# Kernel optimization log

Hardware: AMD Instinct MI355X
Metric: run time of the kernel (lower is better)

The kernel has to match this reference:

```python
import jax, jax.numpy as jnp
import numpy as np

NUM_PER_PATH = 16
MARGIN_INTRA = 0.1
MARGIN_INTER = 1.0


def setup_inputs() -> dict:
    key = jax.random.key(0)
    # [B, block_num, 1, 1, 2]; trailing dims must multiply to 2 (see _get_center view)
    path_fea = jax.random.normal(key, (131072, 64, 1, 1, 2), dtype=jnp.float32)
    return {"path_fea": path_fea}


def reference(path_fea):
    B, block = path_fea.shape[0], path_fea.shape[1]
    D = block * 2                     # flattened per-sample feature dim
    G = B // NUM_PER_PATH             # number of centers (groups)
    fea = path_fea.reshape(B, D)      # [B, D] (matches path_fea[j].view(-1))

    # center: mean over the NUM_PER_PATH samples of each group, per block
    # (identical math to the permute/view dance in _get_center)
    grouped = fea.reshape(G, NUM_PER_PATH, D)          # [G, P, D]
    center = jnp.mean(grouped, axis=1)                 # [G, D]

    # ---- inter loss: hinge on pairwise euclidean distances between centers ----
    sq = jnp.sum(center * center, axis=1)              # [G]
    gram = center @ center.T                           # [G, G]
    d2 = jnp.maximum(sq[:, None] + sq[None, :] - 2.0 * gram, 0.0)
    pair_mask = jnp.triu(jnp.ones((G, G), dtype=bool), k=1)  # i < j
    d = jnp.sqrt(jnp.where(pair_mask, d2, 1.0))        # safe sqrt off-mask
    hinge = jnp.maximum(MARGIN_INTER - d, 0.0) ** 2
    n_pairs = G * (G - 1) / 2.0
    inter_loss = jnp.sum(jnp.where(pair_mask, hinge, 0.0)) / n_pairs

    # ---- intra loss: hinge on distance of each sample to its group center ----
    diff = grouped - center[:, None, :]                # [G, P, D]
    di = jnp.sqrt(jnp.sum(diff * diff, axis=-1))       # [G, P]
    intra_loss = jnp.sum(jnp.maximum(di - MARGIN_INTRA, 0.0) ** 2) / (G * NUM_PER_PATH)

    return (inter_loss, intra_loss)
```

## Files before the change

kernel.cpp:

```cpp
#include <hip/hip_runtime.h>
#include <hip/hip_bf16.h>
#include <math.h>

#define B_ROWS   131072
#define D_DIM    128
#define P_SAMP   16
#define G_GROUPS 8192
#define TILE64   128
#define NTRI     8256
#define K1_BLOCKS (G_GROUPS / 4)

typedef __bf16 bf16x8  __attribute__((ext_vector_type(8)));
typedef float  floatx4 __attribute__((ext_vector_type(4)));
typedef unsigned short u16x8 __attribute__((ext_vector_type(8)));


__device__ __forceinline__ float wave_red64(float v) {
    #pragma unroll
    for (int off = 32; off > 0; off >>= 1) v += __shfl_xor(v, off, 64);
    return v;
}

__global__ __launch_bounds__(256) void k_center_intra(
    const float* __restrict__ x,
    uint2* __restrict__ cfrag,
    float* __restrict__ sq,
    float* __restrict__ partial,
    float* __restrict__ acc)
{
    const int wave = threadIdx.x >> 6;
    const int lane = threadIdx.x & 63;
    const int half = lane >> 5;
    const int c    = lane & 31;
    const int g    = blockIdx.x * 4 + wave;

    if (blockIdx.x == 0 && threadIdx.x == 0) acc[0] = 0.f;

    const float* base = x + (size_t)g * (P_SAMP * D_DIM) + half * D_DIM + c * 4;

    floatx4 v[8];
    #pragma unroll
    for (int l = 0; l < 8; ++l)
        v[l] = *(const floatx4*)(base + l * (2 * D_DIM));

    floatx4 cs = v[0];
    #pragma unroll
    for (int l = 1; l < 8; ++l) cs += v[l];
    #pragma unroll
    for (int k = 0; k < 4; ++k) cs[k] += __shfl_xor(cs[k], 32, 64);
    floatx4 ctr = cs * (1.0f / P_SAMP);

    float p[9];
    #pragma unroll
    for (int l = 0; l < 8; ++l) {
        floatx4 d = v[l] - ctr;
        p[l] = d[0]*d[0] + d[1]*d[1] + d[2]*d[2] + d[3]*d[3];
    }
    p[8] = ctr[0]*ctr[0] + ctr[1]*ctr[1] + ctr[2]*ctr[2] + ctr[3]*ctr[3];

    #pragma unroll
    for (int off = 16; off > 0; off >>= 1) {
        #pragma unroll
        for (int s = 0; s < 9; ++s) p[s] += __shfl_xor(p[s], off, 64);
    }

    if (half == 0) {
        unsigned int b0 = __builtin_bit_cast(unsigned short, (__bf16)ctr[0]);
        unsigned int b1 = __builtin_bit_cast(unsigned short, (__bf16)ctr[1]);
        unsigned int b2 = __builtin_bit_cast(unsigned short, (__bf16)ctr[2]);
        unsigned int b3 = __builtin_bit_cast(unsigned short, (__bf16)ctr[3]);
        uint2 pk;
        pk.x = (b1 << 16) | b0;
        pk.y = (b3 << 16) | b2;
        const int gran = (g >> 4) * 256 + (c >> 1) * 16 + (g & 15);
        cfrag[gran * 2 + (c & 1)] = pk;
    }
    if (lane == 0) sq[g] = p[8];

    float isum = 0.f;
    #pragma unroll
    for (int l = 0; l < 8; ++l) {
        float d = sqrtf(p[l]);
        float t = fmaxf(d - 0.1f, 0.f);
        isum += t * t;
    }
    isum += __shfl_xor(isum, 32, 64);

    __shared__ float sh[4];
    if (lane == 0) sh[wave] = isum;
    __syncthreads();
    if (threadIdx.x == 0)
        partial[blockIdx.x] = sh[0] + sh[1] + sh[2] + sh[3];
}

__global__ __launch_bounds__(256) void k_inter(
    const u16x8* __restrict__ cfrag,
    const float* __restrict__ sq,
    float* __restrict__ acc)
{
    const int wid  = blockIdx.x * 4 + (threadIdx.x >> 6);
    const int lane = threadIdx.x & 63;
    const int lrow = lane & 15;
    const int quad = lane >> 4;

    double s = sqrt(128.5 * 128.5 - 2.0 * (double)wid);
    int ti = (int)(128.5 - s);
    if (ti < 0) ti = 0;
    if (ti > TILE64 - 1) ti = TILE64 - 1;
    #define TRI_OFF(i) ((i) * TILE64 - (((i) * ((i) - 1)) >> 1))
    while (ti > 0 && TRI_OFF(ti) > wid) --ti;
    while (ti < TILE64 - 1 && TRI_OFF(ti + 1) <= wid) ++ti;
    const int tj = ti + (wid - TRI_OFF(ti));
    #undef TRI_OFF

    const int i0 = ti * 64;
    const int j0 = tj * 64;

    floatx4 sqi[4];
    float   sqj[4];
    #pragma unroll
    for (int mt = 0; mt < 4; ++mt)
        sqi[mt] = *(const floatx4*)(sq + i0 + mt * 16 + quad * 4);
    #pragma unroll
    for (int nt = 0; nt < 4; ++nt)
        sqj[nt] = sq[j0 + nt * 16 + lrow];

    #define FRAG_IDX(rg, ks) ((rg) * 256 + ((ks) * 4 + quad) * 16 + lrow)

    bf16x8 a[2][4], b[2][4];
    #pragma unroll
    for (int pb = 0; pb < 2; ++pb) {
        #pragma unroll
        for (int mt = 0; mt < 4; ++mt)
            a[pb][mt] = __builtin_bit_cast(bf16x8, cfrag[FRAG_IDX(ti * 4 + mt, pb)]);
        #pragma unroll
        for (int nt = 0; nt < 4; ++nt)
            b[pb][nt] = __builtin_bit_cast(bf16x8, cfrag[FRAG_IDX(tj * 4 + nt, pb)]);
    }

    floatx4 c4[4][4] = {};

    #pragma unroll
    for (int ks = 0; ks < 4; ++ks) {
        const int cur = ks & 1;
        #pragma unroll
        for (int mt = 0; mt < 4; ++mt)
            #pragma unroll
            for (int nt = 0; nt < 4; ++nt)
                c4[mt][nt] = __builtin_amdgcn_mfma_f32_16x16x32_bf16(
                                a[cur][mt], b[cur][nt], c4[mt][nt], 0, 0, 0);
        if (ks < 2) {
            #pragma unroll
            for (int mt = 0; mt < 4; ++mt)
                a[cur][mt] = __builtin_bit_cast(bf16x8,
                                 cfrag[FRAG_IDX(ti * 4 + mt, ks + 2)]);
            #pragma unroll
            for (int nt = 0; nt < 4; ++nt)
                b[cur][nt] = __builtin_bit_cast(bf16x8,
                                 cfrag[FRAG_IDX(tj * 4 + nt, ks + 2)]);
        }
    }
    #undef FRAG_IDX

    const bool diag = (ti == tj);
    float hsum = 0.f;
    #pragma unroll
    for (int mt = 0; mt < 4; ++mt) {
        #pragma unroll
        for (int nt = 0; nt < 4; ++nt) {
            const int ib = i0 + mt * 16 + quad * 4;
            const int j  = j0 + nt * 16 + lrow;
            #pragma unroll
            for (int r = 0; r < 4; ++r) {
                if (diag && j <= ib + r) continue;
                float d2 = sqi[mt][r] + sqj[nt] - 2.0f * c4[mt][nt][r];
                if (d2 < 1.0f) {
                    float d = sqrtf(fmaxf(d2, 0.f));
                    float t = 1.0f - d;
                    hsum += t * t;
                }
            }
        }
    }
    if (__ballot(hsum != 0.f)) {
        hsum = wave_red64(hsum);
        if (lane == 0) atomicAdd(acc, hsum);
    }
}

__global__ __launch_bounds__(256) void k_final(
    const float* __restrict__ acc,
    const float* __restrict__ partial,
    float* __restrict__ out)
{
    __shared__ float sh[4];
    float s = 0.f;
    for (int i = threadIdx.x; i < K1_BLOCKS; i += 256) s += partial[i];
    s = wave_red64(s);
    const int wave = threadIdx.x >> 6;
    const int lane = threadIdx.x & 63;
    if (lane == 0) sh[wave] = s;
    __syncthreads();
    if (threadIdx.x == 0) {
        const float n_pairs = (float)G_GROUPS * (float)(G_GROUPS - 1) * 0.5f;
        out[0] = acc[0] / n_pairs;
        out[1] = (sh[0] + sh[1] + sh[2] + sh[3]) / (float)B_ROWS;
    }
}

extern "C" void kernel_launch(void* const* d_in, const int* in_sizes, int n_in,
                              void* d_out, int out_size, void* d_ws, size_t ws_size,
                              hipStream_t stream) {
    const float* x = (const float*)d_in[0];
    float* out = (float*)d_out;

    float* acc     = (float*)d_ws;
    float* partial = (float*)((char*)d_ws + 256);
    float* sq      = (float*)((char*)d_ws + 16384);
    uint2* cfrag   = (uint2*)((char*)d_ws + 65536);

    k_center_intra<<<K1_BLOCKS, 256, 0, stream>>>(x, cfrag, sq, partial, acc);

    k_inter<<<NTRI / 4, 256, 0, stream>>>((const u16x8*)cfrag, sq, acc);

    k_final<<<1, 256, 0, stream>>>(acc, partial, out);
}
```

Measured before the change: 116.1 us.

## Stage 128x128 center tiles in LDS shared by four waves in inter kernel

```diff
diff --git a/kernel.cpp b/kernel.cpp
--- a/kernel.cpp
+++ b/kernel.cpp
@@ -6,8 +6,8 @@
 #define D_DIM    128
 #define P_SAMP   16
 #define G_GROUPS 8192
-#define TILE64   128
-#define NTRI     8256
+#define T128     64
+#define NTRI2    2080
 #define K1_BLOCKS (G_GROUPS / 4)
 
 typedef __bf16 bf16x8  __attribute__((ext_vector_type(8)));
@@ -98,23 +98,42 @@
     const float* __restrict__ sq,
     float* __restrict__ acc)
 {
-    const int wid  = blockIdx.x * 4 + (threadIdx.x >> 6);
-    const int lane = threadIdx.x & 63;
+    __shared__ u16x8 smem[4096];
+
+    const int bid = blockIdx.x;
+    float sf = sqrtf(64.5f * 64.5f - 2.0f * (float)bid);
+    int ti = (int)(64.5f - sf);
+    if (ti < 0) ti = 0;
+    if (ti > T128 - 1) ti = T128 - 1;
+    #define TRI_OFF(i) ((i) * T128 - (((i) * ((i) - 1)) >> 1))
+    while (ti > 0 && TRI_OFF(ti) > bid) --ti;
+    while (ti < T128 - 1 && TRI_OFF(ti + 1) <= bid) ++ti;
+    const int tj = ti + (bid - TRI_OFF(ti));
+    #undef TRI_OFF
+
+    const int t = threadIdx.x;
+    const size_t abase = (size_t)ti * 2048;
+    const size_t bbase = (size_t)tj * 2048;
+    #pragma unroll
+    for (int it = 0; it < 8; ++it) {
+        const int idx = t + it * 256;
+        smem[idx]        = cfrag[abase + idx];
+        smem[idx + 2048] = cfrag[bbase + idx];
+    }
+    __syncthreads();
+
+    const int wave = t >> 6;
+    const int lane = t & 63;
+    const int wr   = wave >> 1;
+    const int wc   = wave & 1;
     const int lrow = lane & 15;
     const int quad = lane >> 4;
 
-    double s = sqrt(128.5 * 128.5 - 2.0 * (double)wid);
-    int ti = (int)(128.5 - s);
-    if (ti < 0) ti = 0;
-    if (ti > TILE64 - 1) ti = TILE64 - 1;
-    #define TRI_OFF(i) ((i) * TILE64 - (((i) * ((i) - 1)) >> 1))
-    while (ti > 0 && TRI_OFF(ti) > wid) --ti;
-    while (ti < TILE64 - 1 && TRI_OFF(ti + 1) <= wid) ++ti;
-    const int tj = ti + (wid - TRI_OFF(ti));
-    #undef TRI_OFF
-
-    const int i0 = ti * 64;
-    const int j0 = tj * 64;
+    const bool bdiag = (ti == tj);
+    if (bdiag && wr > wc) return;
+
+    const int i0 = ti * 128 + wr * 64;
+    const int j0 = tj * 128 + wc * 64;
 
     floatx4 sqi[4];
     float   sqj[4];
@@ -125,44 +144,27 @@
     for (int nt = 0; nt < 4; ++nt)
         sqj[nt] = sq[j0 + nt * 16 + lrow];
 
-    #define FRAG_IDX(rg, ks) ((rg) * 256 + ((ks) * 4 + quad) * 16 + lrow)
-
-    bf16x8 a[2][4], b[2][4];
-    #pragma unroll
-    for (int pb = 0; pb < 2; ++pb) {
+    floatx4 c4[4][4] = {};
+
+    #pragma unroll
+    for (int ks = 0; ks < 4; ++ks) {
+        const int go = (ks * 4 + quad) * 16 + lrow;
+        bf16x8 a[4], b[4];
         #pragma unroll
         for (int mt = 0; mt < 4; ++mt)
-            a[pb][mt] = __builtin_bit_cast(bf16x8, cfrag[FRAG_IDX(ti * 4 + mt, pb)]);
+            a[mt] = __builtin_bit_cast(bf16x8, smem[(wr * 4 + mt) * 256 + go]);
         #pragma unroll
         for (int nt = 0; nt < 4; ++nt)
-            b[pb][nt] = __builtin_bit_cast(bf16x8, cfrag[FRAG_IDX(tj * 4 + nt, pb)]);
-    }
-
-    floatx4 c4[4][4] = {};
-
-    #pragma unroll
-    for (int ks = 0; ks < 4; ++ks) {
-        const int cur = ks & 1;
+            b[nt] = __builtin_bit_cast(bf16x8, smem[2048 + (wc * 4 + nt) * 256 + go]);
         #pragma unroll
         for (int mt = 0; mt < 4; ++mt)
             #pragma unroll
             for (int nt = 0; nt < 4; ++nt)
                 c4[mt][nt] = __builtin_amdgcn_mfma_f32_16x16x32_bf16(
-                                a[cur][mt], b[cur][nt], c4[mt][nt], 0, 0, 0);
-        if (ks < 2) {
-            #pragma unroll
-            for (int mt = 0; mt < 4; ++mt)
-                a[cur][mt] = __builtin_bit_cast(bf16x8,
-                                 cfrag[FRAG_IDX(ti * 4 + mt, ks + 2)]);
-            #pragma unroll
-            for (int nt = 0; nt < 4; ++nt)
-                b[cur][nt] = __builtin_bit_cast(bf16x8,
-                                 cfrag[FRAG_IDX(tj * 4 + nt, ks + 2)]);
-        }
-    }
-    #undef FRAG_IDX
-
-    const bool diag = (ti == tj);
+                                a[mt], b[nt], c4[mt][nt], 0, 0, 0);
+    }
+
+    const bool qdiag = (bdiag && wr == wc);
     float hsum = 0.f;
     #pragma unroll
     for (int mt = 0; mt < 4; ++mt) {
@@ -172,12 +174,12 @@
             const int j  = j0 + nt * 16 + lrow;
             #pragma unroll
             for (int r = 0; r < 4; ++r) {
-                if (diag && j <= ib + r) continue;
+                if (qdiag && j <= ib + r) continue;
                 float d2 = sqi[mt][r] + sqj[nt] - 2.0f * c4[mt][nt][r];
                 if (d2 < 1.0f) {
                     float d = sqrtf(fmaxf(d2, 0.f));
-                    float t = 1.0f - d;
-                    hsum += t * t;
+                    float tt = 1.0f - d;
+                    hsum += tt * tt;
                 }
             }
         }
@@ -221,7 +223,7 @@
 
     k_center_intra<<<K1_BLOCKS, 256, 0, stream>>>(x, cfrag, sq, partial, acc);
 
-    k_inter<<<NTRI / 4, 256, 0, stream>>>((const u16x8*)cfrag, sq, acc);
+    k_inter<<<NTRI2, 256, 0, stream>>>((const u16x8*)cfrag, sq, acc);
 
     k_final<<<1, 256, 0, stream>>>(acc, partial, out);
 }
```

Measured after the change: 120.3 us. 1.04x slower.
